# Optimization experiments

Hardware: AMD Instinct MI355X
Metric: run time of the kernel (lower is better)

## Reference

```python
import jax, jax.numpy as jnp
import numpy as np

B, L, D, H = 2, 2048, 2048, 16
HD = D // H          # head_dim = 128
LAT = HD // 4        # latent_dim = 32


def setup_inputs() -> dict:
    key = jax.random.key(0)
    ks = jax.random.split(key, 16)
    def w(k, shape, fan_in):
        return jax.random.normal(k, shape, jnp.float32) / np.float32(np.sqrt(fan_in))
    x = jax.random.normal(ks[0], (B, L, D), jnp.float32)
    # RoPE frequencies, stored as (cos, sin) pairs: [L, HD//2, 2]
    inv_freq = 1.0 / (10000.0 ** (np.arange(0, HD, 2, dtype=np.float32) / HD))
    ang = np.outer(np.arange(L, dtype=np.float32), inv_freq)
    freqs_cis = jnp.stack([jnp.asarray(np.cos(ang)), jnp.asarray(np.sin(ang))], axis=-1)
    return dict(
        x=x, freqs_cis=freqs_cis,
        Wq=w(ks[1], (D, D), D), bq=jnp.zeros((D,), jnp.float32),
        Wk=w(ks[2], (D, D), D), bk=jnp.zeros((D,), jnp.float32),
        Wv=w(ks[3], (D, D), D), bv=jnp.zeros((D,), jnp.float32),
        Wqc=w(ks[4], (LAT, HD), HD), bqc=jnp.zeros((LAT,), jnp.float32),
        Wkc=w(ks[5], (LAT, HD), HD), bkc=jnp.zeros((LAT,), jnp.float32),
        Wvc=w(ks[6], (LAT, HD), HD), bvc=jnp.zeros((LAT,), jnp.float32),
        Wd=w(ks[7], (HD, LAT), LAT), bd=jnp.zeros((HD,), jnp.float32),
        Wo=w(ks[8], (D, D), D), bo=jnp.zeros((D,), jnp.float32),
    )


def _rope(t, freqs_cis):
    # t: [B,H,L,HD]; freqs_cis: [L, HD//2, 2] (cos, sin)
    tp = t.reshape(t.shape[:-1] + (HD // 2, 2))
    a, b = tp[..., 0], tp[..., 1]
    cr = freqs_cis[:, :, 0]  # [L, HD//2]
    ci = freqs_cis[:, :, 1]
    ra = a * cr - b * ci
    rb = a * ci + b * cr
    return jnp.stack([ra, rb], axis=-1).reshape(t.shape)


def reference(x, freqs_cis, Wq, bq, Wk, bk, Wv, bv, Wqc, bqc, Wkc, bkc, Wvc, bvc, Wd, bd, Wo, bo):
    Bx, Lx, Dx = x.shape
    # QKV projections -> [B,H,L,HD]
    def proj(W, bias):
        return (x @ W.T + bias).reshape(Bx, Lx, H, HD).transpose(0, 2, 1, 3)
    q = proj(Wq, bq)
    k = proj(Wk, bk)
    v = proj(Wv, bv)
    q = _rope(q, freqs_cis)
    k = _rope(k, freqs_cis)
    # per-head compression to latent dim: [B,H,L,LAT]
    qc = q @ Wqc.T + bqc
    kc = k @ Wkc.T + bkc
    vc = v @ Wvc.T + bvc
    scores = jnp.einsum('bhie,bhje->bhij', qc, kc) / np.float32(np.sqrt(LAT))
    mask = jnp.triu(jnp.ones((Lx, Lx), bool), 1)  # future positions
    scores = jnp.where(mask, jnp.float32(-jnp.inf), scores)
    probs = jax.nn.softmax(scores, axis=-1)
    attn = jnp.einsum('bhij,bhje->bhie', probs, vc)  # [B,H,L,LAT]
    attn = attn @ Wd.T + bd                          # decompress -> [B,H,L,HD]
    attn = attn.transpose(0, 2, 1, 3).reshape(Bx, Lx, Dx)
    return attn @ Wo.T + bo
```

## Files before the change

### kernel.cpp

```cpp
#include <hip/hip_runtime.h>

typedef __attribute__((ext_vector_type(8))) __bf16 bf16x8;
typedef __attribute__((ext_vector_type(4))) __bf16 bf16x4;
typedef __attribute__((ext_vector_type(4))) float f32x4;
typedef __attribute__((ext_vector_type(16))) float f32x16;

#define LL 2048
#define DD 2048
#define HH 16
#define HDIM 128

__global__ __launch_bounds__(256)
void cvt_all(const float* __restrict__ x, const float* __restrict__ Wq,
             const float* __restrict__ Wk, const float* __restrict__ Wqc,
             const float* __restrict__ Wkc,
             __bf16* __restrict__ xb, __bf16* __restrict__ Wqb, __bf16* __restrict__ Wkb,
             __bf16* __restrict__ Wqcb, __bf16* __restrict__ Wkcb)
{
    size_t i = (size_t)blockIdx.x * 256 + threadIdx.x;
    const float* s; __bf16* d; size_t off;
    if (i < 2097152)      { s = x;   d = xb;   off = i; }
    else if (i < 3145728) { s = Wq;  d = Wqb;  off = i - 2097152; }
    else if (i < 4194304) { s = Wk;  d = Wkb;  off = i - 3145728; }
    else if (i < 4195328) { s = Wqc; d = Wqcb; off = i - 4194304; }
    else                  { s = Wkc; d = Wkcb; off = i - 4195328; }
    float4 v = *(const float4*)(s + off * 4);
    bf16x4 o = { (__bf16)v.x, (__bf16)v.y, (__bf16)v.z, (__bf16)v.w };
    *(bf16x4*)(d + off * 4) = o;
}

__global__ __launch_bounds__(256)
void build_wv_eff(const float* __restrict__ Wv, const float* __restrict__ Wvc,
                  const float* __restrict__ bv, const float* __restrict__ bvc,
                  __bf16* __restrict__ Wveff, float* __restrict__ bveff)
{
    __shared__ float WvcT[128][32];
    const int h = blockIdx.x, dc = blockIdx.y, tid = threadIdx.x;
    for (int i = tid; i < 4096; i += 256) WvcT[i & 127][i >> 7] = Wvc[i];
    __syncthreads();
    const int d  = dc * 64 + (tid & 63);
    const int o0 = (tid >> 6) * 8;
    float acc[8] = {};
    for (int j = 0; j < 128; ++j) {
        const float w = Wv[(size_t)(h * 128 + j) * 2048 + d];
        #pragma unroll
        for (int o = 0; o < 8; ++o) acc[o] += WvcT[j][o0 + o] * w;
    }
    #pragma unroll
    for (int o = 0; o < 8; ++o)
        Wveff[(size_t)(h * 32 + o0 + o) * 2048 + d] = (__bf16)acc[o];
    if (dc == 0 && tid < 32) {
        float s = bvc[tid];
        for (int j = 0; j < 128; ++j) s += WvcT[j][tid] * bv[h * 128 + j];
        bveff[h * 32 + tid] = s;
    }
}

__global__ __launch_bounds__(256)
void build_wo_eff(const float* __restrict__ Wo, const float* __restrict__ Wd,
                  __bf16* __restrict__ Woeff)
{
    __shared__ float WdL[128][32];
    const int dc = blockIdx.x, h = blockIdx.y, tid = threadIdx.x;
    for (int i = tid; i < 4096; i += 256) WdL[i >> 5][i & 31] = Wd[i];
    __syncthreads();
    const int dout = dc * 64 + (tid & 63);
    const int o0   = (tid >> 6) * 8;
    float acc[8] = {};
    const float* wrow = Wo + (size_t)dout * 2048 + h * 128;
    for (int u = 0; u < 128; ++u) {
        const float w = wrow[u];
        #pragma unroll
        for (int o = 0; o < 8; ++o) acc[o] += WdL[u][o0 + o] * w;
    }
    #pragma unroll
    for (int o = 0; o < 8; ++o)
        Woeff[(size_t)dout * 512 + h * 32 + o0 + o] = (__bf16)acc[o];
}

__global__ __launch_bounds__(256)
void build_bo_eff(const float* __restrict__ Wo, const float* __restrict__ bd,
                  const float* __restrict__ bo, float* __restrict__ boeff)
{
    __shared__ float bdL[128];
    const int tid = threadIdx.x;
    if (tid < 128) bdL[tid] = bd[tid];
    __syncthreads();
    const int d  = blockIdx.x * 32 + (tid >> 3);
    const int s0 = (tid & 7) * 64;
    float s = 0.f;
    const float* wrow = Wo + (size_t)d * 2048 + s0 * 4;
    for (int c4 = 0; c4 < 64; ++c4) {
        float4 wv = *(const float4*)(wrow + c4 * 4);
        const int cb = ((s0 + c4) * 4) & 127;
        s += wv.x * bdL[cb] + wv.y * bdL[cb + 1] + wv.z * bdL[cb + 2] + wv.w * bdL[cb + 3];
    }
    #pragma unroll
    for (int off = 4; off; off >>= 1) s += __shfl_down(s, off, 8);
    if ((tid & 7) == 0) boeff[d] = bo[d] + s;
}

typedef unsigned int u32;
typedef const __attribute__((address_space(1))) u32* gp_t;
typedef __attribute__((address_space(3))) u32* lp_t;
__device__ __forceinline__ void gload16(const __bf16* g, __bf16* l)
{
    __builtin_amdgcn_global_load_lds((gp_t)(const void*)g, (lp_t)(void*)l, 16, 0, 0);
}

#define MF16(a, b, c) __builtin_amdgcn_mfma_f32_16x16x32_bf16(a, b, c, 0, 0, 0)

__global__ __launch_bounds__(256, 2)
void gemm_qkv(const __bf16* __restrict__ A,
              const __bf16* __restrict__ Wq, const __bf16* __restrict__ Wk,
              const __bf16* __restrict__ Wveff,
              const float* __restrict__ bq, const float* __restrict__ bk,
              const float* __restrict__ bveff,
              const __bf16* __restrict__ Wqcb, const __bf16* __restrict__ Wkcb,
              const float* __restrict__ bqc, const float* __restrict__ bkc,
              const float* __restrict__ fc,
              __bf16* __restrict__ qc, __bf16* __restrict__ kc, __bf16* __restrict__ vt)
{
    __shared__ __bf16 lds[3][12288];

    const int bid = blockIdx.x;
    const int xcd = bid & 7;
    const int j   = bid >> 3;
    const int bx  = j >> 2;
    const int byl = j & 3;
    const int by  = xcd * 4 + byl;
    const int m0  = by * 128;
    const int which = (bx >= 16) ? 2 : (bx >> 3);
    const int n0  = (which == 2) ? (bx - 16) * 256 : (bx & 7) * 256;
    const __bf16* W = which == 0 ? Wq : which == 1 ? Wk : Wveff;

    const int tid  = threadIdx.x;
    const int wid  = tid >> 6;
    const int lane = tid & 63;
    const int wr   = wid >> 1;
    const int wc   = wid & 1;
    const int l15  = lane & 15;
    const int l4   = lane >> 4;
    const int swz  = (l4 ^ (l15 & 3) ^ ((l15 >> 2) & 3)) * 8;

    const int srl  = lane >> 2;
    const int scol = ((lane & 3) ^ (srl & 3) ^ ((srl >> 2) & 3)) * 8;
    const __bf16* gA0 = A + (size_t)(m0 + wid * 32 + srl) * 2048 + scol;
    const __bf16* gB0 = W + (size_t)(n0 + wid * 64 + srl) * 2048 + scol;

    #define STAGE(bb, kk)                                                \
    {   __bf16* dA = &lds[bb][wid * 1024];                               \
        __bf16* dB = &lds[bb][4096 + wid * 2048];                        \
        gload16(gA0 + (kk), dA);                                         \
        gload16(gA0 + (size_t)16 * 2048 + (kk), dA + 512);               \
        gload16(gB0 + (kk), dB);                                         \
        gload16(gB0 + (size_t)16 * 2048 + (kk), dB + 512);               \
        gload16(gB0 + (size_t)32 * 2048 + (kk), dB + 1024);              \
        gload16(gB0 + (size_t)48 * 2048 + (kk), dB + 1536);              \
    }
    #define RD_A(bb, mf) (*(const bf16x8*)&lds[bb][(wr * 64 + (mf) * 16 + l15) * 32 + swz])
    #define RD_B(bb, nf) (*(const bf16x8*)&lds[bb][4096 + (wc * 128 + (nf) * 16 + l15) * 32 + swz])

    f32x4 acc[4][8] = {};

    STAGE(0, 0) STAGE(1, 32)
    asm volatile("s_waitcnt vmcnt(6)" ::: "memory");
    __builtin_amdgcn_s_barrier();

    #define TB(RB, SB, VM, DOST, kk)                                          \
    {                                                                         \
        bf16x8 fa[4], fb[8];                                                  \
        fa[0] = RD_A(RB, 0); fa[1] = RD_A(RB, 1);                             \
        fa[2] = RD_A(RB, 2); fa[3] = RD_A(RB, 3);                             \
        fb[0] = RD_B(RB, 0); fb[1] = RD_B(RB, 1);                             \
        fb[2] = RD_B(RB, 2); fb[3] = RD_B(RB, 3);                             \
        fb[4] = RD_B(RB, 4); fb[5] = RD_B(RB, 5);                             \
        fb[6] = RD_B(RB, 6); fb[7] = RD_B(RB, 7);                             \
        if (DOST) STAGE(SB, kk)                                               \
        asm volatile("s_waitcnt lgkmcnt(0)" ::: "memory");                    \
        __builtin_amdgcn_sched_barrier(0);                                    \
        __builtin_amdgcn_s_setprio(1);                                        \
        _Pragma("unroll")                                                     \
        for (int mf = 0; mf < 4; ++mf)                                        \
            _Pragma("unroll")                                                 \
            for (int nf = 0; nf < 8; ++nf)                                    \
                acc[mf][nf] = MF16(fa[mf], fb[nf], acc[mf][nf]);              \
        __builtin_amdgcn_s_setprio(0);                                        \
        asm volatile("s_waitcnt vmcnt(" VM ")" ::: "memory");                 \
        __builtin_amdgcn_s_barrier();                                         \
    }

    for (int tt = 0; tt < 60; tt += 3) {
        const int kk = (tt + 2) * 32;
        TB(0, 2, "6", true, kk)
        TB(1, 0, "6", true, kk + 32)
        TB(2, 1, "6", true, kk + 64)
    }
    TB(0, 2, "6", true, 62 * 32)
    TB(1, 0, "6", true, 63 * 32)
    TB(2, 0, "0", false, 0)
    TB(0, 0, "0", false, 0)
    #undef TB
    #undef STAGE
    #undef RD_A
    #undef RD_B

    if (which < 2) {
        __bf16* qt = &lds[0][0];
        const float* bb_ = which ? bk : bq;
        const __bf16* Wb = which ? Wkcb : Wqcb;
        const float*  bs = which ? bkc : bqc;
        const int o   = lane & 31;
        const int hi  = lane >> 5;
        const int b   = m0 >> 11;
        const int l0b = m0 & 2047;
        const int lrow = wid * 32 + o;
        const int l    = l0b + lrow;
        const float* fcr = fc + (size_t)l * 128;
        const float QSCALE = 0.17677669529663689f * 1.44269504088896340f;
        __bf16* outp = which ? kc : qc;

        bf16x8 wf[8];
        #pragma unroll
        for (int ks = 0; ks < 8; ++ks)
            wf[ks] = *(const bf16x8*)(Wb + o * 128 + ks * 16 + hi * 8);

        #pragma unroll
        for (int half = 0; half < 2; ++half) {
            if (wc == half) {
                #pragma unroll
                for (int nf = 0; nf < 8; ++nf) {
                    const int col = nf * 16 + l15;
                    const float bv = bb_[n0 + half * 128 + col];
                    #pragma unroll
                    for (int mf = 0; mf < 4; ++mf) {
                        const int row0 = wr * 64 + mf * 16 + l4 * 4;
                        #pragma unroll
                        for (int rr = 0; rr < 4; ++rr)
                            qt[(row0 + rr) * 136 + col] = (__bf16)(acc[mf][nf][rr] + bv);
                    }
                }
            }
            __syncthreads();

            const int h = (n0 >> 7) + half;
            f32x16 C = {};
            #pragma unroll
            for (int ks = 0; ks < 8; ++ks) {
                bf16x8 af = *(const bf16x8*)&qt[lrow * 136 + ks * 16 + hi * 8];
                const float4 cA = *(const float4*)(fcr + (ks * 8 + hi * 4) * 2);
                const float4 cB = *(const float4*)(fcr + (ks * 8 + hi * 4) * 2 + 4);
                float a, b_;
                a = (float)af[0]; b_ = (float)af[1];
                af[0] = (__bf16)(a * cA.x - b_ * cA.y); af[1] = (__bf16)(a * cA.y + b_ * cA.x);
                a = (float)af[2]; b_ = (float)af[3];
                af[2] = (__bf16)(a * cA.z - b_ * cA.w); af[3] = (__bf16)(a * cA.w + b_ * cA.z);
                a = (float)af[4]; b_ = (float)af[5];
                af[4] = (__bf16)(a * cB.x - b_ * cB.y); af[5] = (__bf16)(a * cB.y + b_ * cB.x);
                a = (float)af[6]; b_ = (float)af[7];
                af[6] = (__bf16)(a * cB.z - b_ * cB.w); af[7] = (__bf16)(a * cB.w + b_ * cB.z);
                C = __builtin_amdgcn_mfma_f32_32x32x16_bf16(af, wf[ks], C, 0, 0, 0);
            }

            const float bias = bs[o];
            const size_t g0row = (size_t)(b * 16 + h) * 2048 + l0b + wid * 32;
            #pragma unroll
            for (int r = 0; r < 16; ++r) {
                const int ro = (r & 3) + 8 * (r >> 2) + 4 * hi;
                float v = C[r] + bias;
                if (which == 0) v *= QSCALE;
                outp[(g0row + ro) * 32 + o] = (__bf16)v;
            }
            __syncthreads();
        }
    } else {
        #pragma unroll
        for (int nf = 0; nf < 8; ++nf) {
            const int ncol = n0 + wc * 128 + nf * 16 + l15;
            const float bv = bveff[ncol];
            const int hh = ncol >> 5, oo = ncol & 31;
            #pragma unroll
            for (int mf = 0; mf < 4; ++mf) {
                const int row0 = m0 + wr * 64 + mf * 16 + l4 * 4;
                const int b = row0 >> 11, l0 = row0 & 2047;
                bf16x4 pk = { (__bf16)(acc[mf][nf][0] + bv), (__bf16)(acc[mf][nf][1] + bv),
                              (__bf16)(acc[mf][nf][2] + bv), (__bf16)(acc[mf][nf][3] + bv) };
                *(bf16x4*)(vt + ((size_t)((b * 16 + hh) * 32 + oo)) * 2048 + l0) = pk;
            }
        }
    }
}

__global__ __launch_bounds__(256)
void gemm_ao(const __bf16* __restrict__ ao, const __bf16* __restrict__ Woeff,
             const float* __restrict__ boeff, float* __restrict__ out)
{
    __shared__ __bf16 As[128][64];
    __shared__ __bf16 Bs[128][64];
    const int bid = blockIdx.x;
    const int x   = bid & 7;
    const int jj  = bid >> 3;
    const int bx  = x * 2 + (jj & 1);
    const int by  = jj >> 1;
    const int m0  = by * 128;
    const int n0  = bx * 128;

    const int tid  = threadIdx.x;
    const int wave = tid >> 6;
    const int lane = tid & 63;
    const int wr   = (wave >> 1) * 64;
    const int wc   = (wave & 1) * 64;
    const int lr   = lane & 15;
    const int lk   = (lane >> 4) * 8;
    const int srow = wave * 32 + (lane >> 3);
    const int scol = (lane & 7) * 8;

    f32x4 acc[4][4] = {};
    __bf16* lA = &As[wave * 32][0];
    __bf16* lB = &Bs[wave * 32][0];
    const __bf16* Ww = Woeff + (size_t)(n0 + srow) * 512 + scol;

    for (int k0 = 0; k0 < 512; k0 += 64) {
        const int kk = k0 + scol;
        const int hblk = kk >> 5, oo = kk & 31;
        #pragma unroll
        for (int j = 0; j < 4; ++j) {
            const int r = m0 + srow + j * 8;
            const int b = r >> 11, l = r & 2047;
            gload16(ao + ((size_t)((b << 4) + hblk) * 2048 + l) * 32 + oo, lA + j * 512);
            gload16(Ww + (size_t)(j * 8) * 512 + k0, lB + j * 512);
        }
        __syncthreads();
        #pragma unroll
        for (int ks = 0; ks < 2; ++ks) {
            bf16x8 af[4], bfr[4];
            #pragma unroll
            for (int m = 0; m < 4; ++m)
                af[m] = *(const bf16x8*)(&As[wr + m * 16 + lr][ks * 32 + lk]);
            #pragma unroll
            for (int n = 0; n < 4; ++n)
                bfr[n] = *(const bf16x8*)(&Bs[wc + n * 16 + lr][ks * 32 + lk]);
            #pragma unroll
            for (int m = 0; m < 4; ++m)
                #pragma unroll
                for (int n = 0; n < 4; ++n)
                    acc[m][n] = MF16(af[m], bfr[n], acc[m][n]);
        }
        __syncthreads();
    }

    const int orow = (lane >> 4) * 4;
    #pragma unroll
    for (int n = 0; n < 4; ++n) {
        const int col = n0 + wc + n * 16 + lr;
        const float bv = boeff[col];
        #pragma unroll
        for (int m = 0; m < 4; ++m) {
            #pragma unroll
            for (int r = 0; r < 4; ++r) {
                const int row = m0 + wr + m * 16 + orow + r;
                out[(size_t)row * 2048 + col] = acc[m][n][r] + bv;
            }
        }
    }
}

__device__ __forceinline__ unsigned pkbf2(float a, float b)
{
    union { __bf16 h[2]; unsigned u; } x;
    x.h[0] = (__bf16)a; x.h[1] = (__bf16)b;
    return x.u;
}

#if __has_builtin(__builtin_amdgcn_permlane32_swap)
typedef unsigned int uint2v __attribute__((ext_vector_type(2)));
__device__ __forceinline__ void plswap(unsigned a, unsigned b, unsigned& w_lo, unsigned& w_hi, int)
{
    uint2v r = __builtin_amdgcn_permlane32_swap(a, b, false, false);
    w_lo = r[0]; w_hi = r[1];
}
#else
__device__ __forceinline__ void plswap(unsigned a, unsigned b, unsigned& w_lo, unsigned& w_hi, int hi)
{
    unsigned ax = (unsigned)__shfl_xor((int)a, 32);
    unsigned bx = (unsigned)__shfl_xor((int)b, 32);
    w_lo = hi ? bx : a;
    w_hi = hi ? b  : ax;
}
#endif

__global__ __launch_bounds__(64)
void attn_part(const __bf16* __restrict__ qc, const __bf16* __restrict__ kc,
               const __bf16* __restrict__ vt,
               float* __restrict__ pm, float* __restrict__ pl, float* __restrict__ po)
{
    const int id  = blockIdx.x;
    const int bhl = id & 7;
    const int c   = id >> 3;
    const int bhh = c / 160;
    const int lin = c - bhh * 160;
    int s, ci;
    if (lin < 16)      { s = lin; ci = 0; }
    else if (lin < 48) { int q = lin - 16; s = 16 + (q >> 1); ci = q & 1; }
    else if (lin < 96) { int q = lin - 48; int d = q / 3; s = 32 + d; ci = q - d * 3; }
    else               { int q = lin - 96; s = 48 + (q >> 2); ci = q & 3; }
    const int bh = bhh * 8 + bhl;

    const int lane = threadIdx.x;
    const int qcol = lane & 31;
    const int hi   = lane >> 5;

    const __bf16* qbase = qc + ((size_t)bh * LL + (size_t)s * 32) * 32;
    const __bf16* kbase = kc + (size_t)bh * LL * 32;
    const __bf16* vbase = vt + (size_t)bh * 32 * LL;

    const bf16x8 qf0 = *(const bf16x8*)(qbase + qcol * 32 + hi * 8);
    const bf16x8 qf1 = *(const bf16x8*)(qbase + qcol * 32 + 16 + hi * 8);

    float m = -1e30f, lsum = 0.f;
    f32x16 O = {};

    const int t0 = ci * 16;
    const int t1 = min(s, t0 + 15);

    const __bf16* krow = kbase + (size_t)(t0 * 32 + qcol) * 32 + hi * 8;
    const __bf16* vrow = vbase + (size_t)qcol * LL + t0 * 32 + hi * 8;
    bf16x8 kc0 = *(const bf16x8*)(krow);
    bf16x8 kc1 = *(const bf16x8*)(krow + 16);
    bf16x8 vc0 = *(const bf16x8*)(vrow);
    bf16x8 vc1 = *(const bf16x8*)(vrow + 16);

    for (int t = t0; t <= t1; ++t) {
        const int tn = (t < t1) ? t + 1 : t;
        const __bf16* krn = kbase + (size_t)(tn * 32 + qcol) * 32 + hi * 8;
        const __bf16* vrn = vbase + (size_t)qcol * LL + tn * 32 + hi * 8;
        bf16x8 kn0 = *(const bf16x8*)(krn);
        bf16x8 kn1 = *(const bf16x8*)(krn + 16);
        bf16x8 vn0 = *(const bf16x8*)(vrn);
        bf16x8 vn1 = *(const bf16x8*)(vrn + 16);

        f32x16 S = {};
        S = __builtin_amdgcn_mfma_f32_32x32x16_bf16(kc0, qf0, S, 0, 0, 0);
        S = __builtin_amdgcn_mfma_f32_32x32x16_bf16(kc1, qf1, S, 0, 0, 0);

        if (t == s) {
            #pragma unroll
            for (int r = 0; r < 16; ++r) {
                const int kl = (r & 3) + 8 * (r >> 2) + 4 * hi;
                if (kl > qcol) S[r] = -1e30f;
            }
        }
        float tm = S[0];
        #pragma unroll
        for (int r = 1; r < 16; ++r) tm = fmaxf(tm, S[r]);
        tm = fmaxf(tm, __shfl_xor(tm, 32));
        const float mn = fmaxf(m, tm);
        const float fr = exp2f(m - mn);
        m = mn;
        float p[16]; float ls = 0.f;
        #pragma unroll
        for (int r = 0; r < 16; ++r) { p[r] = exp2f(S[r] - m); ls += p[r]; }
        lsum = lsum * fr + ls;
        #pragma unroll
        for (int r = 0; r < 16; ++r) O[r] *= fr;

        unsigned w[8];
        #pragma unroll
        for (int i = 0; i < 8; ++i) w[i] = pkbf2(p[2 * i], p[2 * i + 1]);
        union PF { unsigned u[4]; bf16x8 v; } pf1, pf2;
        plswap(w[0], w[2], pf1.u[0], pf1.u[2], hi);
        plswap(w[1], w[3], pf1.u[1], pf1.u[3], hi);
        plswap(w[4], w[6], pf2.u[0], pf2.u[2], hi);
        plswap(w[5], w[7], pf2.u[1], pf2.u[3], hi);

        O = __builtin_amdgcn_mfma_f32_32x32x16_bf16(vc0, pf1.v, O, 0, 0, 0);
        O = __builtin_amdgcn_mfma_f32_32x32x16_bf16(vc1, pf2.v, O, 0, 0, 0);

        kc0 = kn0; kc1 = kn1; vc0 = vn0; vc1 = vn1;
    }

    const float L = lsum + __shfl_xor(lsum, 32);
    const size_t g = (size_t)bh * LL + (size_t)s * 32 + qcol;
    const size_t slot = g * 4 + ci;
    if (hi == 0) { pm[slot] = m; pl[slot] = L; }
    float* pp = po + slot * 32;
    #pragma unroll
    for (int g4 = 0; g4 < 4; ++g4) {
        float4 v = { O[g4 * 4 + 0], O[g4 * 4 + 1], O[g4 * 4 + 2], O[g4 * 4 + 3] };
        *(float4*)(pp + g4 * 8 + 4 * hi) = v;
    }
}

__global__ __launch_bounds__(256)
void attn_comb(const float* __restrict__ pm, const float* __restrict__ pl,
               const float* __restrict__ po, __bf16* __restrict__ ao)
{
    const int g = blockIdx.x * 256 + threadIdx.x;
    const int i = g & (LL - 1);
    const int nch = (i >> 9) + 1;
    float m = -1e30f;
    for (int c = 0; c < nch; ++c) m = fmaxf(m, pm[(size_t)g * 4 + c]);
    float L = 0.f;
    float o[32] = {};
    for (int c = 0; c < nch; ++c) {
        const float w = exp2f(pm[(size_t)g * 4 + c] - m);
        L += w * pl[(size_t)g * 4 + c];
        const float* pp = po + ((size_t)g * 4 + c) * 32;
        #pragma unroll
        for (int d4 = 0; d4 < 8; ++d4) {
            float4 v = *(const float4*)(pp + d4 * 4);
            o[d4*4+0] += w * v.x; o[d4*4+1] += w * v.y;
            o[d4*4+2] += w * v.z; o[d4*4+3] += w * v.w;
        }
    }
    const float inv = 1.f / L;
    #pragma unroll
    for (int d8 = 0; d8 < 4; ++d8) {
        bf16x8 v;
        #pragma unroll
        for (int j = 0; j < 8; ++j) v[j] = (__bf16)(o[d8 * 8 + j] * inv);
        *(bf16x8*)(ao + (size_t)g * 32 + d8 * 8) = v;
    }
}

extern "C" void kernel_launch(void* const* d_in, const int* in_sizes, int n_in,
                              void* d_out, int out_size, void* d_ws, size_t ws_size,
                              hipStream_t stream)
{
    const float* x   = (const float*)d_in[0];
    const float* fc  = (const float*)d_in[1];
    const float* Wq  = (const float*)d_in[2];
    const float* bq  = (const float*)d_in[3];
    const float* Wk  = (const float*)d_in[4];
    const float* bk  = (const float*)d_in[5];
    const float* Wv  = (const float*)d_in[6];
    const float* bv  = (const float*)d_in[7];
    const float* Wqc = (const float*)d_in[8];
    const float* bqc = (const float*)d_in[9];
    const float* Wkc = (const float*)d_in[10];
    const float* bkc = (const float*)d_in[11];
    const float* Wvc = (const float*)d_in[12];
    const float* bvc = (const float*)d_in[13];
    const float* Wd  = (const float*)d_in[14];
    const float* bd  = (const float*)d_in[15];
    const float* Wo  = (const float*)d_in[16];
    const float* bo  = (const float*)d_in[17];
    float* out = (float*)d_out;

    const size_t MB = 1048576;
    char* w = (char*)d_ws;
    __bf16* xb    = (__bf16*)(w);
    __bf16* Wqb   = (__bf16*)(w + 16 * MB);
    __bf16* Wkb   = (__bf16*)(w + 24 * MB);
    __bf16* Wveff = (__bf16*)(w + 32 * MB);
    __bf16* qcbf  = (__bf16*)(w + 66 * MB);
    __bf16* kcbf  = (__bf16*)(w + 70 * MB);
    __bf16* vtbf  = (__bf16*)(w + 74 * MB);
    __bf16* aobf  = (__bf16*)(w + 78 * MB);
    __bf16* Wqcb  = (__bf16*)(w + 82 * MB);
    __bf16* Wkcb  = (__bf16*)(w + 82 * MB + 8192);
    __bf16* Woeff = (__bf16*)(w + 83 * MB);
    float*  boeff = (float*)(w + 85 * MB);
    float*  bveff = (float*)(w + 85 * MB + 8192);

    float* po = (float*)d_ws;
    float* pm = (float*)(w + 32 * MB);
    float* pl = (float*)(w + 33 * MB);

    if (ws_size < (size_t)90 * MB) return;

    cvt_all<<<16392, 256, 0, stream>>>(x, Wq, Wk, Wqc, Wkc, xb, Wqb, Wkb, Wqcb, Wkcb);
    build_wv_eff<<<dim3(16, 32), 256, 0, stream>>>(Wv, Wvc, bv, bvc, Wveff, bveff);
    build_wo_eff<<<dim3(32, 16), 256, 0, stream>>>(Wo, Wd, Woeff);
    build_bo_eff<<<64, 256, 0, stream>>>(Wo, bd, bo, boeff);

    gemm_qkv<<<576, 256, 0, stream>>>(xb, Wqb, Wkb, Wveff, bq, bk, bveff,
                                      Wqcb, Wkcb, bqc, bkc, fc, qcbf, kcbf, vtbf);

    attn_part<<<5120, 64, 0, stream>>>(qcbf, kcbf, vtbf, pm, pl, po);
    attn_comb<<<256, 256, 0, stream>>>(pm, pl, po, aobf);

    gemm_ao<<<512, 256, 0, stream>>>(aobf, Woeff, boeff, out);
}
```

Baseline: 229.4 us.

## Merge setup kernels, triple-buffer gemm_ao, pack four attention waves per block

The four weight-preparation kernels become one launch that picks its role from the block index, which cuts launch overhead. gemm_ao is rewritten with a three-stage LDS ring using 32-wide k-steps, XOR-swizzled LDS addresses to avoid bank conflicts, explicit waitcnt/barrier scheduling, setprio around the MFMA block, and an occupancy hint of 3 blocks per CU. attn_part now runs four independent 64-lane work items per 256-thread block instead of one per block. The changes add complexity and rely on hand-tuned vmcnt values, and the merged setup kernel's shared-memory size applies to the cheap conversion blocks too.

```diff
diff --git a/kernel.cpp b/kernel.cpp
--- a/kernel.cpp
+++ b/kernel.cpp
@@ -11,82 +11,84 @@
 #define HDIM 128
 
 __global__ __launch_bounds__(256)
-void cvt_all(const float* __restrict__ x, const float* __restrict__ Wq,
-             const float* __restrict__ Wk, const float* __restrict__ Wqc,
-             const float* __restrict__ Wkc,
-             __bf16* __restrict__ xb, __bf16* __restrict__ Wqb, __bf16* __restrict__ Wkb,
-             __bf16* __restrict__ Wqcb, __bf16* __restrict__ Wkcb)
-{
-    size_t i = (size_t)blockIdx.x * 256 + threadIdx.x;
-    const float* s; __bf16* d; size_t off;
-    if (i < 2097152)      { s = x;   d = xb;   off = i; }
-    else if (i < 3145728) { s = Wq;  d = Wqb;  off = i - 2097152; }
-    else if (i < 4194304) { s = Wk;  d = Wkb;  off = i - 3145728; }
-    else if (i < 4195328) { s = Wqc; d = Wqcb; off = i - 4194304; }
-    else                  { s = Wkc; d = Wkcb; off = i - 4195328; }
-    float4 v = *(const float4*)(s + off * 4);
-    bf16x4 o = { (__bf16)v.x, (__bf16)v.y, (__bf16)v.z, (__bf16)v.w };
-    *(bf16x4*)(d + off * 4) = o;
-}
-
-__global__ __launch_bounds__(256)
-void build_wv_eff(const float* __restrict__ Wv, const float* __restrict__ Wvc,
-                  const float* __restrict__ bv, const float* __restrict__ bvc,
-                  __bf16* __restrict__ Wveff, float* __restrict__ bveff)
-{
-    __shared__ float WvcT[128][32];
-    const int h = blockIdx.x, dc = blockIdx.y, tid = threadIdx.x;
-    for (int i = tid; i < 4096; i += 256) WvcT[i & 127][i >> 7] = Wvc[i];
-    __syncthreads();
-    const int d  = dc * 64 + (tid & 63);
-    const int o0 = (tid >> 6) * 8;
-    float acc[8] = {};
-    for (int j = 0; j < 128; ++j) {
-        const float w = Wv[(size_t)(h * 128 + j) * 2048 + d];
-        #pragma unroll
-        for (int o = 0; o < 8; ++o) acc[o] += WvcT[j][o0 + o] * w;
-    }
-    #pragma unroll
-    for (int o = 0; o < 8; ++o)
-        Wveff[(size_t)(h * 32 + o0 + o) * 2048 + d] = (__bf16)acc[o];
-    if (dc == 0 && tid < 32) {
-        float s = bvc[tid];
-        for (int j = 0; j < 128; ++j) s += WvcT[j][tid] * bv[h * 128 + j];
-        bveff[h * 32 + tid] = s;
-    }
-}
-
-__global__ __launch_bounds__(256)
-void build_wo_eff(const float* __restrict__ Wo, const float* __restrict__ Wd,
-                  __bf16* __restrict__ Woeff)
-{
-    __shared__ float WdL[128][32];
-    const int dc = blockIdx.x, h = blockIdx.y, tid = threadIdx.x;
-    for (int i = tid; i < 4096; i += 256) WdL[i >> 5][i & 31] = Wd[i];
-    __syncthreads();
-    const int dout = dc * 64 + (tid & 63);
-    const int o0   = (tid >> 6) * 8;
-    float acc[8] = {};
-    const float* wrow = Wo + (size_t)dout * 2048 + h * 128;
-    for (int u = 0; u < 128; ++u) {
-        const float w = wrow[u];
-        #pragma unroll
-        for (int o = 0; o < 8; ++o) acc[o] += WdL[u][o0 + o] * w;
-    }
-    #pragma unroll
-    for (int o = 0; o < 8; ++o)
-        Woeff[(size_t)dout * 512 + h * 32 + o0 + o] = (__bf16)acc[o];
-}
-
-__global__ __launch_bounds__(256)
-void build_bo_eff(const float* __restrict__ Wo, const float* __restrict__ bd,
-                  const float* __restrict__ bo, float* __restrict__ boeff)
-{
-    __shared__ float bdL[128];
+void setup_all(const float* __restrict__ x, const float* __restrict__ Wq,
+               const float* __restrict__ Wk, const float* __restrict__ Wqc,
+               const float* __restrict__ Wkc,
+               const float* __restrict__ Wv, const float* __restrict__ Wvc,
+               const float* __restrict__ bv, const float* __restrict__ bvc,
+               const float* __restrict__ Wo, const float* __restrict__ Wd,
+               const float* __restrict__ bd, const float* __restrict__ bo,
+               __bf16* __restrict__ xb, __bf16* __restrict__ Wqb, __bf16* __restrict__ Wkb,
+               __bf16* __restrict__ Wqcb, __bf16* __restrict__ Wkcb,
+               __bf16* __restrict__ Wveff, float* __restrict__ bveff,
+               __bf16* __restrict__ Woeff, float* __restrict__ boeff)
+{
+    __shared__ float sm[128 * 32];
     const int tid = threadIdx.x;
+    const int bid = blockIdx.x;
+
+    if (bid < 16392) {
+        size_t i = (size_t)bid * 256 + tid;
+        const float* s; __bf16* d; size_t off;
+        if (i < 2097152)      { s = x;   d = xb;   off = i; }
+        else if (i < 3145728) { s = Wq;  d = Wqb;  off = i - 2097152; }
+        else if (i < 4194304) { s = Wk;  d = Wkb;  off = i - 3145728; }
+        else if (i < 4195328) { s = Wqc; d = Wqcb; off = i - 4194304; }
+        else                  { s = Wkc; d = Wkcb; off = i - 4195328; }
+        float4 v = *(const float4*)(s + off * 4);
+        bf16x4 o = { (__bf16)v.x, (__bf16)v.y, (__bf16)v.z, (__bf16)v.w };
+        *(bf16x4*)(d + off * 4) = o;
+        return;
+    }
+    int idx = bid - 16392;
+    if (idx < 512) {
+        float (*WvcT)[32] = (float(*)[32])sm;
+        const int h = idx >> 5, dc = idx & 31;
+        for (int i = tid; i < 4096; i += 256) WvcT[i & 127][i >> 7] = Wvc[i];
+        __syncthreads();
+        const int d  = dc * 64 + (tid & 63);
+        const int o0 = (tid >> 6) * 8;
+        float acc[8] = {};
+        for (int jj = 0; jj < 128; ++jj) {
+            const float w = Wv[(size_t)(h * 128 + jj) * 2048 + d];
+            #pragma unroll
+            for (int o = 0; o < 8; ++o) acc[o] += WvcT[jj][o0 + o] * w;
+        }
+        #pragma unroll
+        for (int o = 0; o < 8; ++o)
+            Wveff[(size_t)(h * 32 + o0 + o) * 2048 + d] = (__bf16)acc[o];
+        if (dc == 0 && tid < 32) {
+            float s = bvc[tid];
+            for (int jj = 0; jj < 128; ++jj) s += WvcT[jj][tid] * bv[h * 128 + jj];
+            bveff[h * 32 + tid] = s;
+        }
+        return;
+    }
+    idx -= 512;
+    if (idx < 512) {
+        float (*WdL)[32] = (float(*)[32])sm;
+        const int dc = idx & 31, h = idx >> 5;
+        for (int i = tid; i < 4096; i += 256) WdL[i >> 5][i & 31] = Wd[i];
+        __syncthreads();
+        const int dout = dc * 64 + (tid & 63);
+        const int o0   = (tid >> 6) * 8;
+        float acc[8] = {};
+        const float* wrow = Wo + (size_t)dout * 2048 + h * 128;
+        for (int u = 0; u < 128; ++u) {
+            const float w = wrow[u];
+            #pragma unroll
+            for (int o = 0; o < 8; ++o) acc[o] += WdL[u][o0 + o] * w;
+        }
+        #pragma unroll
+        for (int o = 0; o < 8; ++o)
+            Woeff[(size_t)dout * 512 + h * 32 + o0 + o] = (__bf16)acc[o];
+        return;
+    }
+    idx -= 512;
+    float* bdL = sm;
     if (tid < 128) bdL[tid] = bd[tid];
     __syncthreads();
-    const int d  = blockIdx.x * 32 + (tid >> 3);
+    const int d  = idx * 32 + (tid >> 3);
     const int s0 = (tid & 7) * 64;
     float s = 0.f;
     const float* wrow = Wo + (size_t)d * 2048 + s0 * 4;
@@ -291,12 +293,11 @@
     }
 }
 
-__global__ __launch_bounds__(256)
+__global__ __launch_bounds__(256, 3)
 void gemm_ao(const __bf16* __restrict__ ao, const __bf16* __restrict__ Woeff,
              const float* __restrict__ boeff, float* __restrict__ out)
 {
-    __shared__ __bf16 As[128][64];
-    __shared__ __bf16 Bs[128][64];
+    __shared__ __bf16 lds[3][2][4096];
     const int bid = blockIdx.x;
     const int x   = bid & 7;
     const int jj  = bid >> 3;
@@ -306,61 +307,86 @@
     const int n0  = bx * 128;
 
     const int tid  = threadIdx.x;
-    const int wave = tid >> 6;
+    const int wid  = tid >> 6;
     const int lane = tid & 63;
-    const int wr   = (wave >> 1) * 64;
-    const int wc   = (wave & 1) * 64;
-    const int lr   = lane & 15;
-    const int lk   = (lane >> 4) * 8;
-    const int srow = wave * 32 + (lane >> 3);
-    const int scol = (lane & 7) * 8;
+    const int wr   = wid >> 1;
+    const int wc   = wid & 1;
+    const int l15  = lane & 15;
+    const int l4   = lane >> 4;
+    const int swz  = (l4 ^ (l15 & 3) ^ ((l15 >> 2) & 3)) * 8;
+
+    const int srl  = lane >> 2;
+    const int scol = ((lane & 3) ^ (srl & 3) ^ ((srl >> 2) & 3)) * 8;
+    const int r0   = m0 + wid * 32 + srl;
+    const int b0   = r0 >> 11, li0 = r0 & 2047;
+    const __bf16* gA0 = ao + ((size_t)(b0 << 4) * 2048 + li0) * 32 + scol;
+    const __bf16* gA1 = ao + ((size_t)(b0 << 4) * 2048 + li0 + 16) * 32 + scol;
+    const __bf16* gB0 = Woeff + (size_t)(n0 + wid * 32 + srl) * 512 + scol;
+
+    #define STAGE(bb, kk)                                                     \
+    {   __bf16* dA = &lds[bb][0][wid * 1024];                                 \
+        __bf16* dB = &lds[bb][1][wid * 1024];                                 \
+        const size_t ka = (size_t)((kk) >> 5) * 65536;                        \
+        gload16(gA0 + ka, dA);                                                \
+        gload16(gA1 + ka, dA + 512);                                          \
+        gload16(gB0 + (kk), dB);                                              \
+        gload16(gB0 + (size_t)16 * 512 + (kk), dB + 512);                     \
+    }
+    #define RD_A(bb, mf) (*(const bf16x8*)&lds[bb][0][(wr * 64 + (mf) * 16 + l15) * 32 + swz])
+    #define RD_B(bb, nf) (*(const bf16x8*)&lds[bb][1][(wc * 64 + (nf) * 16 + l15) * 32 + swz])
 
     f32x4 acc[4][4] = {};
-    __bf16* lA = &As[wave * 32][0];
-    __bf16* lB = &Bs[wave * 32][0];
-    const __bf16* Ww = Woeff + (size_t)(n0 + srow) * 512 + scol;
-
-    for (int k0 = 0; k0 < 512; k0 += 64) {
-        const int kk = k0 + scol;
-        const int hblk = kk >> 5, oo = kk & 31;
-        #pragma unroll
-        for (int j = 0; j < 4; ++j) {
-            const int r = m0 + srow + j * 8;
-            const int b = r >> 11, l = r & 2047;
-            gload16(ao + ((size_t)((b << 4) + hblk) * 2048 + l) * 32 + oo, lA + j * 512);
-            gload16(Ww + (size_t)(j * 8) * 512 + k0, lB + j * 512);
-        }
-        __syncthreads();
-        #pragma unroll
-        for (int ks = 0; ks < 2; ++ks) {
-            bf16x8 af[4], bfr[4];
+
+    STAGE(0, 0) STAGE(1, 32)
+    asm volatile("s_waitcnt vmcnt(4)" ::: "memory");
+    __builtin_amdgcn_s_barrier();
+
+    #define TB(RB, SB, VM, DOST, kk)                                          \
+    {                                                                         \
+        bf16x8 fa[4], fb[4];                                                  \
+        fa[0] = RD_A(RB, 0); fa[1] = RD_A(RB, 1);                             \
+        fa[2] = RD_A(RB, 2); fa[3] = RD_A(RB, 3);                             \
+        fb[0] = RD_B(RB, 0); fb[1] = RD_B(RB, 1);                             \
+        fb[2] = RD_B(RB, 2); fb[3] = RD_B(RB, 3);                             \
+        if (DOST) STAGE(SB, kk)                                               \
+        asm volatile("s_waitcnt lgkmcnt(0)" ::: "memory");                    \
+        __builtin_amdgcn_sched_barrier(0);                                    \
+        __builtin_amdgcn_s_setprio(1);                                        \
+        _Pragma("unroll")                                                     \
+        for (int mf = 0; mf < 4; ++mf)                                        \
+            _Pragma("unroll")                                                 \
+            for (int nf = 0; nf < 4; ++nf)                                    \
+                acc[mf][nf] = MF16(fa[mf], fb[nf], acc[mf][nf]);              \
+        __builtin_amdgcn_s_setprio(0);                                        \
+        asm volatile("s_waitcnt vmcnt(" VM ")" ::: "memory");                 \
+        __builtin_amdgcn_s_barrier();                                         \
+    }
+
+    for (int tt = 0; tt < 12; tt += 3) {
+        const int kk = (tt + 2) * 32;
+        TB(0, 2, "4", true, kk)
+        TB(1, 0, "4", true, kk + 32)
+        TB(2, 1, "4", true, kk + 64)
+    }
+    TB(0, 2, "4", true, 14 * 32)
+    TB(1, 0, "4", true, 15 * 32)
+    TB(2, 0, "0", false, 0)
+    TB(0, 0, "0", false, 0)
+    #undef TB
+    #undef STAGE
+    #undef RD_A
+    #undef RD_B
+
+    #pragma unroll
+    for (int nf = 0; nf < 4; ++nf) {
+        const int col = n0 + wc * 64 + nf * 16 + l15;
+        const float bv = boeff[col];
+        #pragma unroll
+        for (int mf = 0; mf < 4; ++mf) {
+            const int row0 = m0 + wr * 64 + mf * 16 + l4 * 4;
             #pragma unroll
-            for (int m = 0; m < 4; ++m)
-                af[m] = *(const bf16x8*)(&As[wr + m * 16 + lr][ks * 32 + lk]);
-            #pragma unroll
-            for (int n = 0; n < 4; ++n)
-                bfr[n] = *(const bf16x8*)(&Bs[wc + n * 16 + lr][ks * 32 + lk]);
-            #pragma unroll
-            for (int m = 0; m < 4; ++m)
-                #pragma unroll
-                for (int n = 0; n < 4; ++n)
-                    acc[m][n] = MF16(af[m], bfr[n], acc[m][n]);
-        }
-        __syncthreads();
-    }
-
-    const int orow = (lane >> 4) * 4;
-    #pragma unroll
-    for (int n = 0; n < 4; ++n) {
-        const int col = n0 + wc + n * 16 + lr;
-        const float bv = boeff[col];
-        #pragma unroll
-        for (int m = 0; m < 4; ++m) {
-            #pragma unroll
-            for (int r = 0; r < 4; ++r) {
-                const int row = m0 + wr + m * 16 + orow + r;
-                out[(size_t)row * 2048 + col] = acc[m][n][r] + bv;
-            }
+            for (int rr = 0; rr < 4; ++rr)
+                out[(size_t)(row0 + rr) * 2048 + col] = acc[mf][nf][rr] + bv;
         }
     }
 }
@@ -389,12 +415,12 @@
 }
 #endif
 
-__global__ __launch_bounds__(64)
+__global__ __launch_bounds__(256)
 void attn_part(const __bf16* __restrict__ qc, const __bf16* __restrict__ kc,
                const __bf16* __restrict__ vt,
                float* __restrict__ pm, float* __restrict__ pl, float* __restrict__ po)
 {
-    const int id  = blockIdx.x;
+    const int id  = blockIdx.x * 4 + (threadIdx.x >> 6);
     const int bhl = id & 7;
     const int c   = id >> 3;
     const int bhh = c / 160;
@@ -406,7 +432,7 @@
     else               { int q = lin - 96; s = 48 + (q >> 2); ci = q & 3; }
     const int bh = bhh * 8 + bhl;
 
-    const int lane = threadIdx.x;
+    const int lane = threadIdx.x & 63;
     const int qcol = lane & 31;
     const int hi   = lane >> 5;
 
@@ -518,7 +544,7 @@
     for (int d8 = 0; d8 < 4; ++d8) {
         bf16x8 v;
         #pragma unroll
-        for (int j = 0; j < 8; ++j) v[j] = (__bf16)(o[d8 * 8 + j] * inv);
+        for (int jj = 0; jj < 8; ++jj) v[jj] = (__bf16)(o[d8 * 8 + jj] * inv);
         *(bf16x8*)(ao + (size_t)g * 32 + d8 * 8) = v;
     }
 }
@@ -569,15 +595,15 @@
 
     if (ws_size < (size_t)90 * MB) return;
 
-    cvt_all<<<16392, 256, 0, stream>>>(x, Wq, Wk, Wqc, Wkc, xb, Wqb, Wkb, Wqcb, Wkcb);
-    build_wv_eff<<<dim3(16, 32), 256, 0, stream>>>(Wv, Wvc, bv, bvc, Wveff, bveff);
-    build_wo_eff<<<dim3(32, 16), 256, 0, stream>>>(Wo, Wd, Woeff);
-    build_bo_eff<<<64, 256, 0, stream>>>(Wo, bd, bo, boeff);
+    setup_all<<<17480, 256, 0, stream>>>(x, Wq, Wk, Wqc, Wkc, Wv, Wvc, bv, bvc,
+                                         Wo, Wd, bd, bo,
+                                         xb, Wqb, Wkb, Wqcb, Wkcb,
+                                         Wveff, bveff, Woeff, boeff);
 
     gemm_qkv<<<576, 256, 0, stream>>>(xb, Wqb, Wkb, Wveff, bq, bk, bveff,
                                       Wqcb, Wkcb, bqc, bkc, fc, qcbf, kcbf, vtbf);
 
-    attn_part<<<5120, 64, 0, stream>>>(qcbf, kcbf, vtbf, pm, pl, po);
+    attn_part<<<1280, 256, 0, stream>>>(qcbf, kcbf, vtbf, pm, pl, po);
     attn_comb<<<256, 256, 0, stream>>>(pm, pl, po, aobf);
 
     gemm_ao<<<512, 256, 0, stream>>>(aobf, Woeff, boeff, out);
```

After: 223.7 us. 1.03x faster.
